# Performance work log

Measured on AMD Instinct MI355X. Metric: run time of the kernel, lower is better.

Reference implementation:

```python
import jax, jax.numpy as jnp
import numpy as np

SCALE = 1.0 / np.sqrt(64.0)  # hard-coded 64**0.5 in original, independent of dims


def setup_inputs() -> dict:
    key = jax.random.key(0)
    k1, k2 = jax.random.split(key)
    x = jax.random.normal(k1, (8, 2048, 1024), dtype=jnp.float32)
    # kernel[0]=W_Q, kernel[1]=W_K, kernel[2]=W_V, each [d_in, d_out]
    kernel = jax.random.normal(k2, (3, 1024, 1024), dtype=jnp.float32) * 0.02
    return {"x": x, "kernel": kernel}


def reference(x, kernel):
    # x: [b, s, d_in], kernel: [3, d_in, d_out]
    wq = jnp.einsum('bsd,de->bse', x, kernel[0])
    wk = jnp.einsum('bsd,de->bse', x, kernel[1])
    wv = jnp.einsum('bsd,de->bse', x, kernel[2])
    scores = jnp.einsum('bqe,bke->bqk', wq, wk) * SCALE  # [b, s, s]
    attn = jax.nn.softmax(scores, axis=-1)
    return jnp.einsum('bqk,bke->bqe', attn, wv)  # [b, s, d_out]
```

## Files before the change

### kernel.cpp

```cpp
#include <hip/hip_runtime.h>
#include <stdint.h>

typedef unsigned short u16;
typedef unsigned short u16x4 __attribute__((ext_vector_type(4)));
typedef unsigned short u16x8 __attribute__((ext_vector_type(8)));
typedef _Float16 f16x8 __attribute__((ext_vector_type(8)));
typedef float f32x4 __attribute__((ext_vector_type(4)));

__device__ __forceinline__ u16 f2h(float f) {
  _Float16 x = (_Float16)f;
  return __builtin_bit_cast(u16, x);
}

__device__ __forceinline__ void gld16(const void* g, void* l) {
  __builtin_amdgcn_global_load_lds(
      (const __attribute__((address_space(1))) unsigned int*)g,
      (__attribute__((address_space(3))) unsigned int*)l,
      16, 0, 0);
}

#define BAR __builtin_amdgcn_s_barrier()
#define SCHEDB __builtin_amdgcn_sched_barrier(0)
#define LGKM0                                        \
  do {                                               \
    asm volatile("s_waitcnt lgkmcnt(0)" ::: "memory"); \
    __builtin_amdgcn_sched_barrier(0);               \
  } while (0)
#define LGKM8 asm volatile("s_waitcnt lgkmcnt(8)" ::: "memory")
#define VM6 asm volatile("s_waitcnt vmcnt(6)" ::: "memory")
#define VM0 asm volatile("s_waitcnt vmcnt(0)" ::: "memory")

#define TBM 256
#define TBN 256
#define TBK 64

template <int QM, int QN>
__device__ __forceinline__ void mfma_quad(f32x4 (&acc)[8][4],
                                          const f16x8 (&ar)[4][2],
                                          const f16x8 (&br)[2][2]) {
#pragma unroll
  for (int kk = 0; kk < 2; ++kk)
#pragma unroll
    for (int mm = 0; mm < 4; ++mm)
#pragma unroll
      for (int nn = 0; nn < 2; ++nn)
        acc[QM * 4 + mm][QN * 2 + nn] = __builtin_amdgcn_mfma_f32_16x16x32_f16(
            ar[mm][kk], br[nn][kk], acc[QM * 4 + mm][QN * 2 + nn], 0, 0, 0);
}

template <int EPI, int XSWZ>
__global__ __launch_bounds__(512, 2) void gemm256(
    const u16* __restrict__ Ap, const u16* __restrict__ Bp,
    void* __restrict__ Cp, float* __restrict__ xtra, int K, int lda, int ldb,
    int ldc, long sA, long sB, long sC) {
  __shared__ char lds[131072];

  const int gx = gridDim.x, gy = gridDim.y;
  int bx, by, z;
  if constexpr (XSWZ == 1) {
    const int p = (blockIdx.z * gy + blockIdx.y) * gx + blockIdx.x;
    z = p & 7;
    const int rest = p >> 3;
    bx = rest % gx;
    by = rest / gx;
  } else {
    const int lin = (blockIdx.z * gy + blockIdx.y) * gx + blockIdx.x;
    const int cpx = (gx * gy * gridDim.z) >> 3;
    const int swz = (lin & 7) * cpx + (lin >> 3);
    bx = swz % gx;
    const int tq = swz / gx;
    by = tq % gy;
    z = tq / gy;
  }

  const int tid = threadIdx.x;
  const int lane = tid & 63, wid = tid >> 6;
  const int wr = wid >> 2, wc = wid & 3;
  const int l15 = lane & 15, l4 = lane >> 4;
  const int bm = by * TBM, bn = bx * TBN;

  const u16* Ag = Ap + (long)z * sA + (long)bm * lda;
  const u16* Bg = Bp + (long)z * sB + (long)bn * ldb;

  const int sw = l15 & 7;
  const int s0 = (l4 ^ sw) * 16, s1 = ((4 + l4) ^ sw) * 16;
  int aB[2][2], bB[2][2];
  aB[0][0] = wr * 16384 + l15 * 128 + s0;
  aB[0][1] = wr * 16384 + l15 * 128 + s1;
  bB[0][0] = 32768 + (wc >> 1) * 16384 + ((wc & 1) * 64 + l15) * 128 + s0;
  bB[0][1] = 32768 + (wc >> 1) * 16384 + ((wc & 1) * 64 + l15) * 128 + s1;
  aB[1][0] = aB[0][0] + 65536;
  aB[1][1] = aB[0][1] + 65536;
  bB[1][0] = bB[0][0] + 65536;
  bB[1][1] = bB[0][1] + 65536;

#define DSA(BUF, QM, AR)                                                     \
  do {                                                                       \
    _Pragma("unroll") for (int mm = 0; mm < 4; ++mm) {                       \
      AR[mm][0] = *(const f16x8*)(lds + aB[BUF][0] + (QM)*8192 + mm * 2048); \
      AR[mm][1] = *(const f16x8*)(lds + aB[BUF][1] + (QM)*8192 + mm * 2048); \
    }                                                                        \
  } while (0)
#define DSB(BUF, QN, BR)                                                     \
  do {                                                                       \
    _Pragma("unroll") for (int nn = 0; nn < 2; ++nn) {                       \
      BR[nn][0] = *(const f16x8*)(lds + bB[BUF][0] + (QN)*4096 + nn * 2048); \
      BR[nn][1] = *(const f16x8*)(lds + bB[BUF][1] + (QN)*4096 + nn * 2048); \
    }                                                                        \
  } while (0)

  const u16 *gpA0[2], *gpA1[2], *gpB0[2], *gpB1[2];
  int loA0[2], loA1[2], loB0[2], loB1[2];
  {
    const u16* bases[4] = {Ag, Ag + 128L * lda, Bg, Bg + 128L * ldb};
    const int lds_[4] = {lda, lda, ldb, ldb};
    const u16** gps[4] = {gpA0, gpA1, gpB0, gpB1};
    int* los[4] = {loA0, loA1, loB0, loB1};
#pragma unroll
    for (int X = 0; X < 4; ++X)
#pragma unroll
      for (int it = 0; it < 2; ++it) {
        int idx = it * 512 + tid, r = idx >> 3, p = idx & 7, s = p ^ (r & 7);
        gps[X][it] = bases[X] + (long)r * lds_[X] + s * 8;
        los[X][it] = X * 16384 + (it * 512 + wid * 64) * 16;
      }
  }
#define STAGE(X, BUF, kt)                                              \
  do {                                                                 \
    long ko = (long)(kt) << 7;                                         \
    gld16((const char*)gp##X[0] + ko, lds + ((BUF)*65536 + lo##X[0])); \
    gld16((const char*)gp##X[1] + ko, lds + ((BUF)*65536 + lo##X[1])); \
  } while (0)

  f32x4 acc[8][4] = {};
  f16x8 a0[4][2], a1[4][2], b0[2][2], b1[2][2];
  const int nk = K / TBK;

  STAGE(A0, 0, 0);
  STAGE(A1, 0, 0);
  STAGE(B0, 0, 0);
  STAGE(B1, 0, 0);
  STAGE(A0, 1, 1);
  STAGE(A1, 1, 1);
  STAGE(B0, 1, 1);
  VM6;
  BAR;
  SCHEDB;

#define TILE(BUF, t)                                                 \
  do {                                                               \
                       \
    DSA(BUF, 0, a0);                                                 \
    DSB(BUF, 0, b0);                                                 \
    if ((t) + 1 < nk) STAGE(B1, BUF ^ 1, (t) + 1);                   \
    LGKM8;                                                           \
    BAR;                                                             \
    LGKM0;                                                           \
    __builtin_amdgcn_s_setprio(1);                                   \
    mfma_quad<0, 0>(acc, a0, b0);                                    \
    __builtin_amdgcn_s_setprio(0);                                   \
    SCHEDB;                                                          \
    BAR;                                                             \
                           \
    DSA(BUF, 1, a1);                                                 \
    if ((t) + 2 < nk) STAGE(A0, BUF, (t) + 2);                       \
    BAR;                                                             \
    LGKM0;                                                           \
    __builtin_amdgcn_s_setprio(1);                                   \
    mfma_quad<1, 0>(acc, a1, b0);                                    \
    __builtin_amdgcn_s_setprio(0);                                   \
    SCHEDB;                                                          \
    BAR;                                                             \
                           \
    DSB(BUF, 1, b1);                                                 \
    if ((t) + 2 < nk) STAGE(A1, BUF, (t) + 2);                       \
    BAR;                                                             \
    LGKM0;                                                           \
    __builtin_amdgcn_s_setprio(1);                                   \
    mfma_quad<0, 1>(acc, a0, b1);                                    \
    __builtin_amdgcn_s_setprio(0);                                   \
    SCHEDB;                                                          \
    BAR;                                                             \
     \
    if ((t) + 2 < nk) {                                              \
      STAGE(B0, BUF, (t) + 2);                                       \
      VM6;                                                           \
    } else if ((t) + 1 < nk) {                                       \
      VM0;                                                           \
    }                                                                \
    BAR;                                                             \
    __builtin_amdgcn_s_setprio(1);                                   \
    mfma_quad<1, 1>(acc, a1, b1);                                    \
    __builtin_amdgcn_s_setprio(0);                                   \
    SCHEDB;                                                          \
    BAR;                                                             \
  } while (0)

  for (int t = 0; t < nk; t += 2) {
    TILE(0, t);
    TILE(1, t + 1);
  }

  if constexpr (EPI == 0) {
    if (bn < 2048) {
      u16* C = (u16*)Cp;
#pragma unroll
      for (int m = 0; m < 8; ++m)
#pragma unroll
        for (int n = 0; n < 4; ++n) {
          int row = bm + wr * 128 + m * 16 + l4 * 4;
          int col = bn + wc * 64 + n * 16 + l15;
#pragma unroll
          for (int r = 0; r < 4; ++r)
            C[(long)(row + r) * ldc + col] = f2h(acc[m][n][r]);
        }
    } else {
#pragma unroll
      for (int m = 0; m < 8; ++m) {
        const int slotk = wr * 16 + m * 2 + (l4 >> 1);
        const int koff8 = (l4 & 1) * 8;
#pragma unroll
        for (int n = 0; n < 4; ++n) {
          const int e = wc * 64 + n * 16 + l15;
          u16x4 pk;
#pragma unroll
          for (int rr = 0; rr < 4; ++rr) pk[rr] = f2h(acc[m][n][rr]);
          *(u16x4*)(lds + e * 512 + ((slotk ^ (e & 31)) << 4) + koff8) = pk;
        }
      }
      __syncthreads();
      u16* Vt = (u16*)xtra;
      const int zz = bm >> 11;
      const int kb = bm & 2047;
      const int er = tid >> 3;
      const int q = tid & 7;
#pragma unroll
      for (int p = 0; p < 4; ++p) {
        const int e = p * 64 + er;
        const char* src = lds + e * 512;
        u16* dst =
            Vt + (long)zz * 2097152 + (long)((bn - 2048) + e) * 2048 + kb;
        const int ex = e & 31;
#pragma unroll
        for (int j = 0; j < 4; ++j) {
          const int c = q + 8 * j;
          u16x8 v = *(const u16x8*)(src + ((c ^ ex) << 4));
          *(u16x8*)(dst + c * 8) = v;
        }
      }
    }
  } else if constexpr (EPI == 1) {
    u16* C = (u16*)Cp + (long)z * sC;
    float* rp = (float*)lds;
#pragma unroll
    for (int m = 0; m < 8; ++m) {
#pragma unroll
      for (int r = 0; r < 4; ++r) {
        const int row = bm + wr * 128 + m * 16 + l4 * 4 + r;
        float ps = 0.f;
#pragma unroll
        for (int n = 0; n < 4; ++n) {
          float p = __expf(acc[m][n][r] * 0.125f - 3.0f);
          C[(long)row * ldc + bn + wc * 64 + n * 16 + l15] = f2h(p);
          ps += p;
        }
#pragma unroll
        for (int d = 1; d < 16; d <<= 1) ps += __shfl_xor(ps, d, 64);
        if (l15 == 0) rp[wc * 256 + wr * 128 + m * 16 + l4 * 4 + r] = ps;
      }
    }
    __syncthreads();
    if (tid < 256) {
      float s = rp[tid] + rp[256 + tid] + rp[512 + tid] + rp[768 + tid];
      xtra[((long)z * 2048 + bm + tid) * 8 + bx] = s;
    }
  } else {
    float* C = (float*)Cp + (long)z * sC;
    float* ivl = (float*)lds;
    if (tid < 256) {
      const float* sp = xtra + ((long)z * 2048 + bm + tid) * 8;
      float s = 0.f;
#pragma unroll
      for (int j = 0; j < 8; ++j) s += sp[j];
      ivl[tid] = 1.0f / s;
    }
    __syncthreads();
#pragma unroll
    for (int m = 0; m < 8; ++m)
#pragma unroll
      for (int r = 0; r < 4; ++r) {
        const int rloc = wr * 128 + m * 16 + l4 * 4 + r;
        const float iv = ivl[rloc];
        const long row = bm + rloc;
#pragma unroll
        for (int n = 0; n < 4; ++n)
          C[row * ldc + bn + wc * 64 + n * 16 + l15] = acc[m][n][r] * iv;
      }
  }
#undef TILE
#undef STAGE
#undef DSA
#undef DSB
}

__global__ __launch_bounds__(256) void prep(const float* __restrict__ x,
                                            const float* __restrict__ w,
                                            u16* __restrict__ xh,
                                            u16* __restrict__ Wt) {
  const int b = blockIdx.x;
  if (b < 768) {
    __shared__ u16 T[64][72];
    const int z = b >> 8, rem = b & 255, by = rem >> 4, bxx = rem & 15;
    const float* ip = w + (long)z * 1048576;
    u16* op = Wt + (long)z * 1048576;
    const int r0 = by * 64, c0 = bxx * 64;
    const int t = threadIdx.x, c8 = t & 7, rr = t >> 3;
#pragma unroll
    for (int h = 0; h < 2; ++h) {
      const int r = rr + h * 32;
      const float* g = ip + (long)(r0 + r) * 1024 + c0 + c8 * 8;
      float4 a = *(const float4*)g;
      float4 bb = *(const float4*)(g + 4);
      u16x8 v;
      v[0] = f2h(a.x); v[1] = f2h(a.y); v[2] = f2h(a.z); v[3] = f2h(a.w);
      v[4] = f2h(bb.x); v[5] = f2h(bb.y); v[6] = f2h(bb.z); v[7] = f2h(bb.w);
      *(u16x8*)&T[r][c8 * 8] = v;
    }
    __syncthreads();
#pragma unroll
    for (int h = 0; h < 2; ++h) {
      const int oc = rr + h * 32;
      u16x8 v;
#pragma unroll
      for (int j = 0; j < 8; ++j) v[j] = T[c8 * 8 + j][oc];
      *(u16x8*)(op + (long)(c0 + oc) * 1024 + r0 + c8 * 8) = v;
    }
  } else {
    long i = (long)(b - 768) * 256 + threadIdx.x;
    const long stride = 2048L * 256;
    for (; i < 2097152L; i += stride) {
      const float* g = x + i * 8;
      float4 a = *(const float4*)g;
      float4 bb = *(const float4*)(g + 4);
      u16x8 o;
      o[0] = f2h(a.x); o[1] = f2h(a.y); o[2] = f2h(a.z); o[3] = f2h(a.w);
      o[4] = f2h(bb.x); o[5] = f2h(bb.y); o[6] = f2h(bb.z); o[7] = f2h(bb.w);
      *(u16x8*)(xh + i * 8) = o;
    }
  }
}

extern "C" void kernel_launch(void* const* d_in, const int* in_sizes, int n_in,
                              void* d_out, int out_size, void* d_ws,
                              size_t ws_size, hipStream_t stream) {
  const float* x = (const float*)d_in[0];
  const float* w = (const float*)d_in[1];
  float* out = (float*)d_out;

  u16* ws = (u16*)d_ws;
  u16* QKV = ws;
  u16* Wt = ws + 50331648L;
  float* Spart = (float*)(ws + 50331648L);
  u16* Vt = ws + 53477376L;
  u16* xh = ws + 70254592L;
  u16* S = ws + 70254592L;

  prep<<<dim3(2816), 256, 0, stream>>>(x, w, xh, Wt);

  gemm256<0, 0><<<dim3(12, 64, 1), 512, 0, stream>>>(
      xh, Wt, (void*)QKV, (float*)Vt, 1024, 1024, 1024, 3072, 0L, 0L, 0L);

  gemm256<1, 1><<<dim3(8, 8, 8), 512, 0, stream>>>(
      QKV, QKV + 1024, (void*)S, Spart, 1024, 3072, 3072, 2048, 6291456L,
      6291456L, 4194304L);

  gemm256<2, 1><<<dim3(4, 8, 8), 512, 0, stream>>>(
      S, Vt, (void*)out, Spart, 2048, 2048, 2048, 1024, 4194304L, 2097152L,
      2097152L);
}
```

Measured before the change: 274.9 us.

## Fuse fp32-to-fp16 conversion of x into QKV projection GEMM A-loads

Removes the separate pass that converted x to fp16 in global memory. The QKV GEMM now loads fp32 x tiles into registers, converts them to fp16 and writes them to LDS inside the pipelined K loop. B keeps using direct global-to-LDS loads. This saves the write and re-read of the 32 MB fp16 copy of x. In exchange it doubles A-side global load bytes per tile, adds register pressure and VALU conversion work, and uses synchronous register staging instead of async LDS loads.

```diff
diff --git a/kernel.cpp b/kernel.cpp
--- a/kernel.cpp
+++ b/kernel.cpp
@@ -28,6 +28,8 @@
   } while (0)
 #define LGKM8 asm volatile("s_waitcnt lgkmcnt(8)" ::: "memory")
 #define VM6 asm volatile("s_waitcnt vmcnt(6)" ::: "memory")
+#define VM4 asm volatile("s_waitcnt vmcnt(4)" ::: "memory")
+#define VM2 asm volatile("s_waitcnt vmcnt(2)" ::: "memory")
 #define VM0 asm volatile("s_waitcnt vmcnt(0)" ::: "memory")
 
 #define TBM 256
@@ -48,9 +50,9 @@
             ar[mm][kk], br[nn][kk], acc[QM * 4 + mm][QN * 2 + nn], 0, 0, 0);
 }
 
-template <int EPI, int XSWZ>
+template <int EPI, int XSWZ, int ASRC>
 __global__ __launch_bounds__(512, 2) void gemm256(
-    const u16* __restrict__ Ap, const u16* __restrict__ Bp,
+    const void* __restrict__ Apv, const u16* __restrict__ Bp,
     void* __restrict__ Cp, float* __restrict__ xtra, int K, int lda, int ldb,
     int ldc, long sA, long sB, long sC) {
   __shared__ char lds[131072];
@@ -79,7 +81,12 @@
   const int l15 = lane & 15, l4 = lane >> 4;
   const int bm = by * TBM, bn = bx * TBN;
 
-  const u16* Ag = Ap + (long)z * sA + (long)bm * lda;
+  const u16* Ag16 = nullptr;
+  const float* Axf = nullptr;
+  if constexpr (ASRC == 0)
+    Ag16 = (const u16*)Apv + (long)z * sA + (long)bm * lda;
+  else
+    Axf = (const float*)Apv + (long)z * sA + (long)bm * lda;
   const u16* Bg = Bp + (long)z * sB + (long)bn * ldb;
 
   const int sw = l15 & 7;
@@ -111,19 +118,23 @@
 
   const u16 *gpA0[2], *gpA1[2], *gpB0[2], *gpB1[2];
   int loA0[2], loA1[2], loB0[2], loB1[2];
-  {
-    const u16* bases[4] = {Ag, Ag + 128L * lda, Bg, Bg + 128L * ldb};
-    const int lds_[4] = {lda, lda, ldb, ldb};
-    const u16** gps[4] = {gpA0, gpA1, gpB0, gpB1};
-    int* los[4] = {loA0, loA1, loB0, loB1};
-#pragma unroll
-    for (int X = 0; X < 4; ++X)
-#pragma unroll
-      for (int it = 0; it < 2; ++it) {
-        int idx = it * 512 + tid, r = idx >> 3, p = idx & 7, s = p ^ (r & 7);
-        gps[X][it] = bases[X] + (long)r * lds_[X] + s * 8;
-        los[X][it] = X * 16384 + (it * 512 + wid * 64) * 16;
-      }
+#pragma unroll
+  for (int it = 0; it < 2; ++it) {
+    const int idx = it * 512 + tid, r = idx >> 3, p = idx & 7;
+    const int s = p ^ (r & 7);
+    gpB0[it] = Bg + (long)r * ldb + s * 8;
+    gpB1[it] = Bg + 128L * ldb + (long)r * ldb + s * 8;
+    loB0[it] = 2 * 16384 + (it * 512 + wid * 64) * 16;
+    loB1[it] = 3 * 16384 + (it * 512 + wid * 64) * 16;
+    if constexpr (ASRC == 0) {
+      gpA0[it] = Ag16 + (long)r * lda + s * 8;
+      gpA1[it] = Ag16 + 128L * lda + (long)r * lda + s * 8;
+      loA0[it] = (it * 512 + wid * 64) * 16;
+      loA1[it] = 16384 + (it * 512 + wid * 64) * 16;
+    } else {
+      gpA0[it] = nullptr; gpA1[it] = nullptr;
+      loA0[it] = 0; loA1[it] = 0;
+    }
   }
 #define STAGE(X, BUF, kt)                                              \
   do {                                                                 \
@@ -132,18 +143,55 @@
     gld16((const char*)gp##X[1] + ko, lds + ((BUF)*65536 + lo##X[1])); \
   } while (0)
 
+  float4 fA[2][2][2];
+#define LOADA(H, kt)                                                       \
+  do {                                                                     \
+    _Pragma("unroll") for (int it = 0; it < 2; ++it) {                     \
+      const int idx = it * 512 + tid, r = idx >> 3, p = idx & 7;           \
+      const int s = p ^ (r & 7);                                           \
+      const float* g = Axf + (long)((H)*128 + r) * lda + (kt)*TBK + s * 8; \
+      fA[H][it][0] = *(const float4*)g;                                    \
+      fA[H][it][1] = *(const float4*)(g + 4);                              \
+    }                                                                      \
+  } while (0)
+#define CVTWRA(H, BUF)                                                    \
+  do {                                                                    \
+    _Pragma("unroll") for (int it = 0; it < 2; ++it) {                    \
+      const int idx = it * 512 + tid;                                     \
+      float4 a_ = fA[H][it][0], b_ = fA[H][it][1];                        \
+      u16x8 o;                                                            \
+      o[0] = f2h(a_.x); o[1] = f2h(a_.y);                                 \
+      o[2] = f2h(a_.z); o[3] = f2h(a_.w);                                 \
+      o[4] = f2h(b_.x); o[5] = f2h(b_.y);                                 \
+      o[6] = f2h(b_.z); o[7] = f2h(b_.w);                                 \
+      *(u16x8*)(lds + (BUF)*65536 + (H)*16384 + idx * 16) = o;            \
+    }                                                                     \
+  } while (0)
+
   f32x4 acc[8][4] = {};
   f16x8 a0[4][2], a1[4][2], b0[2][2], b1[2][2];
   const int nk = K / TBK;
 
-  STAGE(A0, 0, 0);
-  STAGE(A1, 0, 0);
-  STAGE(B0, 0, 0);
-  STAGE(B1, 0, 0);
-  STAGE(A0, 1, 1);
-  STAGE(A1, 1, 1);
-  STAGE(B0, 1, 1);
-  VM6;
+  if constexpr (ASRC == 0) {
+    STAGE(A0, 0, 0);
+    STAGE(A1, 0, 0);
+    STAGE(B0, 0, 0);
+    STAGE(B1, 0, 0);
+    STAGE(A0, 1, 1);
+    STAGE(A1, 1, 1);
+    STAGE(B0, 1, 1);
+    VM6;
+  } else {
+    LOADA(0, 0); VM0; SCHEDB; CVTWRA(0, 0);
+    LOADA(1, 0); VM0; SCHEDB; CVTWRA(1, 0);
+    LOADA(0, 1); VM0; SCHEDB; CVTWRA(0, 1);
+    LOADA(1, 1); VM0; SCHEDB; CVTWRA(1, 1);
+    STAGE(B0, 0, 0);
+    STAGE(B1, 0, 0);
+    STAGE(B0, 1, 1);
+    asm volatile("s_waitcnt lgkmcnt(0)" ::: "memory");
+    VM2;
+  }
   BAR;
   SCHEDB;
 
@@ -163,7 +211,10 @@
     BAR;                                                             \
                            \
     DSA(BUF, 1, a1);                                                 \
-    if ((t) + 2 < nk) STAGE(A0, BUF, (t) + 2);                       \
+    if ((t) + 2 < nk) {                                              \
+      if constexpr (ASRC == 0) { STAGE(A0, BUF, (t) + 2); }          \
+      else { LOADA(0, (t) + 2); }                                    \
+    }                                                                \
     BAR;                                                             \
     LGKM0;                                                           \
     __builtin_amdgcn_s_setprio(1);                                   \
@@ -173,7 +224,15 @@
     BAR;                                                             \
                            \
     DSB(BUF, 1, b1);                                                 \
-    if ((t) + 2 < nk) STAGE(A1, BUF, (t) + 2);                       \
+    if ((t) + 2 < nk) {                                              \
+      if constexpr (ASRC == 0) { STAGE(A1, BUF, (t) + 2); }          \
+      else {                                                         \
+        LOADA(1, (t) + 2);                                           \
+        VM4;                    \
+        SCHEDB;                                                      \
+        CVTWRA(0, BUF);                                              \
+      }                                                              \
+    }                                                                \
     BAR;                                                             \
     LGKM0;                                                           \
     __builtin_amdgcn_s_setprio(1);                                   \
@@ -181,10 +240,16 @@
     __builtin_amdgcn_s_setprio(0);                                   \
     SCHEDB;                                                          \
     BAR;                                                             \
-     \
+               \
     if ((t) + 2 < nk) {                                              \
       STAGE(B0, BUF, (t) + 2);                                       \
-      VM6;                                                           \
+      if constexpr (ASRC == 0) {                                     \
+        VM6;                                                         \
+      } else {                                                       \
+        VM2;                   \
+        SCHEDB;                                                      \
+        CVTWRA(1, BUF);                                              \
+      }                                                              \
     } else if ((t) + 1 < nk) {                                       \
       VM0;                                                           \
     }                                                                \
@@ -301,52 +366,38 @@
 #undef STAGE
 #undef DSA
 #undef DSB
-}
-
-__global__ __launch_bounds__(256) void prep(const float* __restrict__ x,
-                                            const float* __restrict__ w,
-                                            u16* __restrict__ xh,
+#undef LOADA
+#undef CVTWRA
+}
+
+__global__ __launch_bounds__(256) void prep(const float* __restrict__ w,
                                             u16* __restrict__ Wt) {
+  __shared__ u16 T[64][72];
   const int b = blockIdx.x;
-  if (b < 768) {
-    __shared__ u16 T[64][72];
-    const int z = b >> 8, rem = b & 255, by = rem >> 4, bxx = rem & 15;
-    const float* ip = w + (long)z * 1048576;
-    u16* op = Wt + (long)z * 1048576;
-    const int r0 = by * 64, c0 = bxx * 64;
-    const int t = threadIdx.x, c8 = t & 7, rr = t >> 3;
-#pragma unroll
-    for (int h = 0; h < 2; ++h) {
-      const int r = rr + h * 32;
-      const float* g = ip + (long)(r0 + r) * 1024 + c0 + c8 * 8;
-      float4 a = *(const float4*)g;
-      float4 bb = *(const float4*)(g + 4);
-      u16x8 v;
-      v[0] = f2h(a.x); v[1] = f2h(a.y); v[2] = f2h(a.z); v[3] = f2h(a.w);
-      v[4] = f2h(bb.x); v[5] = f2h(bb.y); v[6] = f2h(bb.z); v[7] = f2h(bb.w);
-      *(u16x8*)&T[r][c8 * 8] = v;
-    }
-    __syncthreads();
-#pragma unroll
-    for (int h = 0; h < 2; ++h) {
-      const int oc = rr + h * 32;
-      u16x8 v;
-#pragma unroll
-      for (int j = 0; j < 8; ++j) v[j] = T[c8 * 8 + j][oc];
-      *(u16x8*)(op + (long)(c0 + oc) * 1024 + r0 + c8 * 8) = v;
-    }
-  } else {
-    long i = (long)(b - 768) * 256 + threadIdx.x;
-    const long stride = 2048L * 256;
-    for (; i < 2097152L; i += stride) {
-      const float* g = x + i * 8;
-      float4 a = *(const float4*)g;
-      float4 bb = *(const float4*)(g + 4);
-      u16x8 o;
-      o[0] = f2h(a.x); o[1] = f2h(a.y); o[2] = f2h(a.z); o[3] = f2h(a.w);
-      o[4] = f2h(bb.x); o[5] = f2h(bb.y); o[6] = f2h(bb.z); o[7] = f2h(bb.w);
-      *(u16x8*)(xh + i * 8) = o;
-    }
+  const int z = b >> 8, rem = b & 255, by = rem >> 4, bxx = rem & 15;
+  const float* ip = w + (long)z * 1048576;
+  u16* op = Wt + (long)z * 1048576;
+  const int r0 = by * 64, c0 = bxx * 64;
+  const int t = threadIdx.x, c8 = t & 7, rr = t >> 3;
+#pragma unroll
+  for (int h = 0; h < 2; ++h) {
+    const int r = rr + h * 32;
+    const float* g = ip + (long)(r0 + r) * 1024 + c0 + c8 * 8;
+    float4 a = *(const float4*)g;
+    float4 bb = *(const float4*)(g + 4);
+    u16x8 v;
+    v[0] = f2h(a.x); v[1] = f2h(a.y); v[2] = f2h(a.z); v[3] = f2h(a.w);
+    v[4] = f2h(bb.x); v[5] = f2h(bb.y); v[6] = f2h(bb.z); v[7] = f2h(bb.w);
+    *(u16x8*)&T[r][c8 * 8] = v;
+  }
+  __syncthreads();
+#pragma unroll
+  for (int h = 0; h < 2; ++h) {
+    const int oc = rr + h * 32;
+    u16x8 v;
+#pragma unroll
+    for (int j = 0; j < 8; ++j) v[j] = T[c8 * 8 + j][oc];
+    *(u16x8*)(op + (long)(c0 + oc) * 1024 + r0 + c8 * 8) = v;
   }
 }
 
@@ -362,19 +413,19 @@
   u16* Wt = ws + 50331648L;
   float* Spart = (float*)(ws + 50331648L);
   u16* Vt = ws + 53477376L;
-  u16* xh = ws + 70254592L;
   u16* S = ws + 70254592L;
 
-  prep<<<dim3(2816), 256, 0, stream>>>(x, w, xh, Wt);
-
-  gemm256<0, 0><<<dim3(12, 64, 1), 512, 0, stream>>>(
-      xh, Wt, (void*)QKV, (float*)Vt, 1024, 1024, 1024, 3072, 0L, 0L, 0L);
-
-  gemm256<1, 1><<<dim3(8, 8, 8), 512, 0, stream>>>(
-      QKV, QKV + 1024, (void*)S, Spart, 1024, 3072, 3072, 2048, 6291456L,
-      6291456L, 4194304L);
-
-  gemm256<2, 1><<<dim3(4, 8, 8), 512, 0, stream>>>(
-      S, Vt, (void*)out, Spart, 2048, 2048, 2048, 1024, 4194304L, 2097152L,
-      2097152L);
-}
+  prep<<<dim3(768), 256, 0, stream>>>(w, Wt);
+
+  gemm256<0, 0, 1><<<dim3(12, 64, 1), 512, 0, stream>>>(
+      (const void*)x, Wt, (void*)QKV, (float*)Vt, 1024, 1024, 1024, 3072, 0L,
+      0L, 0L);
+
+  gemm256<1, 1, 0><<<dim3(8, 8, 8), 512, 0, stream>>>(
+      (const void*)QKV, QKV + 1024, (void*)S, Spart, 1024, 3072, 3072, 2048,
+      6291456L, 6291456L, 4194304L);
+
+  gemm256<2, 1, 0><<<dim3(4, 8, 8), 512, 0, stream>>>(
+      (const void*)S, Vt, (void*)out, Spart, 2048, 2048, 2048, 1024, 4194304L,
+      2097152L, 2097152L);
+}
```

Measured after the change: 502.0 us. 1.83x slower.
